# Performance work log

Hardware: AMD Instinct MI355X
Metric: run time of the kernel (lower is better)

Reference implementation:

```python
import jax, jax.numpy as jnp
import numpy as np

DIM = 1280
N_HEADS = 10
HEAD_DIM = 128
BASE = 10000.0
BATCH = 2
SEQ = 2048


def _rope(x):
    # x: [b, h, s, d]; matches source: split even/odd channels, rotate, concat halves
    b, h, s, d = x.shape
    theta = 1.0 / (BASE ** (jnp.arange(0, d, 2, dtype=jnp.float32) / d))  # [d/2]
    ang = jnp.arange(s, dtype=jnp.float32)[:, None] * theta               # [s, d/2]
    cos = jnp.cos(ang)
    sin = jnp.sin(ang)
    x1 = x[..., 0::2]
    x2 = x[..., 1::2]
    return jnp.concatenate([x1 * cos - x2 * sin, x1 * sin + x2 * cos], axis=-1)


def setup_inputs() -> dict:
    key = jax.random.key(0)
    ks = jax.random.split(key, 6)
    w_std = 0.02
    x = jax.random.normal(ks[0], (BATCH, SEQ, DIM), dtype=jnp.float32)
    positions = jnp.arange(SEQ, dtype=jnp.int64 if jax.config.jax_enable_x64 else jnp.int32)
    Wq = jax.random.normal(ks[1], (DIM, DIM), dtype=jnp.float32) * w_std
    Wk = jax.random.normal(ks[2], (DIM, DIM), dtype=jnp.float32) * w_std
    Wv = jax.random.normal(ks[3], (DIM, DIM), dtype=jnp.float32) * w_std
    Wo = jax.random.normal(ks[4], (DIM, DIM), dtype=jnp.float32) * w_std
    bq = jnp.zeros((DIM,), jnp.float32)
    bk = jnp.zeros((DIM,), jnp.float32)
    bv = jnp.zeros((DIM,), jnp.float32)
    bo = jnp.zeros((DIM,), jnp.float32)
    return {"x": x, "positions": positions, "Wq": Wq, "bq": bq, "Wk": Wk,
            "bk": bk, "Wv": Wv, "bv": bv, "Wo": Wo, "bo": bo}


def reference(x, positions, Wq, bq, Wk, bk, Wv, bv, Wo, bo):
    b, s, _ = x.shape
    scale = 1.0 / np.sqrt(HEAD_DIM)

    def proj(W, bias):
        y = jnp.einsum('bsd,ed->bse', x, W) + bias  # Linear: x @ W^T + b
        return y.reshape(b, s, N_HEADS, HEAD_DIM).transpose(0, 2, 1, 3)

    q = _rope(proj(Wq, bq))  # [b, h, s, hd]
    k = _rope(proj(Wk, bk))
    v = proj(Wv, bv)

    scores = jnp.einsum('bhqd,bhkd->bhqk', q, k) * scale
    causal = jnp.tril(jnp.ones((s, s), dtype=bool))
    scores = jnp.where(causal, scores, jnp.float32(-jnp.inf))
    attn = jax.nn.softmax(scores, axis=-1)
    out = jnp.einsum('bhqk,bhkd->bhqd', attn, v)
    out = out.transpose(0, 2, 1, 3).reshape(b, s, N_HEADS * HEAD_DIM)
    return jnp.einsum('bse,de->bsd', out, Wo) + bo
```

## Files before the change

### kernel.cpp

```cpp
#include <hip/hip_runtime.h>
#include <cmath>

typedef unsigned short u16;
typedef __attribute__((ext_vector_type(8))) short bf16x8;
typedef __attribute__((ext_vector_type(4))) float f32x4;

#define B_    2
#define SEQ_  2048
#define NH_   10
#define HD_   128
#define DIM_  1280

__device__ __forceinline__ u16 f2bf(float f) {
    union { float f; unsigned u; } v; v.f = f;
    unsigned r = (v.u + 0x7fffu + ((v.u >> 16) & 1u)) >> 16;
    return (u16)r;
}
__device__ __forceinline__ float bf2f(u16 h) {
    union { unsigned u; float f; } v; v.u = ((unsigned)h) << 16;
    return v.f;
}
__device__ __forceinline__ unsigned cvt2(float lo, float hi) {
    unsigned r;
    asm("v_cvt_pk_bf16_f32 %0, %1, %2" : "=v"(r) : "v"(lo), "v"(hi));
    return r;
}
__device__ __forceinline__ f32x4 mfma16(bf16x8 a, bf16x8 b, f32x4 c) {
    return __builtin_amdgcn_mfma_f32_16x16x32_bf16(a, b, c, 0, 0, 0);
}
__device__ __forceinline__ void g2l16(const void* g, void* l) {
    __builtin_amdgcn_global_load_lds(
        (const __attribute__((address_space(1))) unsigned*)g,
        (__attribute__((address_space(3))) unsigned*)l, 16, 0, 0);
}
__device__ __forceinline__ ushort4 pack4(float a, float b, float c, float d) {
    union { ushort4 w; unsigned u[2]; } r;
    r.u[0] = cvt2(a, b);
    r.u[1] = cvt2(c, d);
    return r.w;
}
__device__ __forceinline__ bf16x8 ldsr128(unsigned byte_off) {
    bf16x8 r;
    asm volatile("ds_read_b128 %0, %1" : "=v"(r) : "v"(byte_off));
    return r;
}
__device__ __forceinline__ unsigned lds_off(const void* p) {
    return (unsigned)(unsigned long long)
        (__attribute__((address_space(3))) const void*)p;
}

#define LGKM0() do { asm volatile("s_waitcnt lgkmcnt(0)" ::: "memory"); \
                     __builtin_amdgcn_sched_barrier(0); } while (0)
#define VMC(n)  asm volatile("s_waitcnt vmcnt(" #n ")" ::: "memory")

__global__ __launch_bounds__(256) void cvt_k(const float* __restrict__ x,
                                             const float* __restrict__ w0,
                                             const float* __restrict__ w1,
                                             const float* __restrict__ w2,
                                             const float* __restrict__ w3,
                                             u16* __restrict__ xb,
                                             u16* __restrict__ d0,
                                             u16* __restrict__ d1,
                                             u16* __restrict__ d2,
                                             u16* __restrict__ d3,
                                             float* __restrict__ ct,
                                             float* __restrict__ st) {
    const int NX = B_ * SEQ_ * DIM_;
    const int WN = DIM_ * DIM_;
    const int NCV = (NX + 4 * WN) / 8 / 256;
    int bid = blockIdx.x;
    if (bid >= NCV) {
        int idx = (bid - NCV) * 256 + threadIdx.x;
        int s = idx >> 6, j = idx & 63;
        float e = (float)j * (1.0f / 64.0f);
        float theta = 1.0f / powf(10000.0f, e);
        float ang = (float)s * theta;
        ct[idx] = cosf(ang);
        st[idx] = sinf(ang);
        return;
    }
    int i = (bid * 256 + threadIdx.x) * 8;
    const float* src; u16* dst; int off;
    if (i < NX) { src = x; dst = xb; off = i; }
    else {
        int j = i - NX; int w = j / WN; off = j - w * WN;
        src = (w == 0) ? w0 : (w == 1) ? w1 : (w == 2) ? w2 : w3;
        dst = (w == 0) ? d0 : (w == 1) ? d1 : (w == 2) ? d2 : d3;
    }
    float4 a0 = *(const float4*)(src + off);
    float4 a1 = *(const float4*)(src + off + 4);
    union { uint4 q; unsigned w[4]; } t;
    t.w[0] = cvt2(a0.x, a0.y);
    t.w[1] = cvt2(a0.z, a0.w);
    t.w[2] = cvt2(a1.x, a1.y);
    t.w[3] = cvt2(a1.z, a1.w);
    *(uint4*)(dst + off) = t.q;
}

template <typename OT>
__device__ __forceinline__ void gemm_core(const u16* __restrict__ A,
                                          const u16* __restrict__ W,
                                          const float* __restrict__ bias,
                                          OT* __restrict__ C,
                                          int m_blk, int n_blk,
                                          u16* As, u16* Bs) {
    const int tid = threadIdx.x;
    const int wave = tid >> 6, lane = tid & 63;
    const int quad = lane >> 4, l16 = lane & 15;
    const int w_m = (wave >> 1) * 64, w_n = (wave & 1) * 64;
    const int srow = wave * 32;
    const int lrow = lane >> 3;
    const int csw = ((lane & 7) ^ lrow) * 8;
    const int rsw = l16 & 7;
    f32x4 acc[4][4] = {};

    const u16* pa = A + (size_t)(m_blk + srow + lrow) * DIM_ + csw;
    const u16* pb = W + (size_t)(n_blk + srow + lrow) * DIM_ + csw;

    for (int k0 = 0; k0 < DIM_; k0 += 64) {
        #pragma unroll
        for (int i = 0; i < 4; ++i) {
            g2l16(pa + k0 + i * 8 * DIM_, As + (srow + i * 8) * 64);
            g2l16(pb + k0 + i * 8 * DIM_, Bs + (srow + i * 8) * 64);
        }
        __syncthreads();
        #pragma unroll
        for (int kk = 0; kk < 2; ++kk) {
            bf16x8 af[4], bf[4];
            #pragma unroll
            for (int mt = 0; mt < 4; ++mt)
                af[mt] = *(const bf16x8*)&As[(w_m + mt * 16 + l16) * 64
                                             + ((kk * 4 + quad) ^ rsw) * 8];
            #pragma unroll
            for (int nt = 0; nt < 4; ++nt)
                bf[nt] = *(const bf16x8*)&Bs[(w_n + nt * 16 + l16) * 64
                                             + ((kk * 4 + quad) ^ rsw) * 8];
            #pragma unroll
            for (int mt = 0; mt < 4; ++mt)
                #pragma unroll
                for (int nt = 0; nt < 4; ++nt)
                    acc[mt][nt] = mfma16(af[mt], bf[nt], acc[mt][nt]);
        }
        __syncthreads();
    }
    #pragma unroll
    for (int nt = 0; nt < 4; ++nt) {
        int col = n_blk + w_n + nt * 16 + l16;
        float bv = bias[col];
        #pragma unroll
        for (int mt = 0; mt < 4; ++mt) {
            #pragma unroll
            for (int r = 0; r < 4; ++r) {
                int row = m_blk + w_m + mt * 16 + quad * 4 + r;
                float v = acc[mt][nt][r] + bv;
                if constexpr (sizeof(OT) == 4) C[(size_t)row * DIM_ + col] = v;
                else C[(size_t)row * DIM_ + col] = (OT)f2bf(v);
            }
        }
    }
}

__device__ __forceinline__ void gemm256_core(const u16* __restrict__ A,
                                             const u16* __restrict__ W,
                                             const float* __restrict__ bias,
                                             u16* __restrict__ C,
                                             int m_blk, int n_blk,
                                             u16* sm) {
    const int tid = threadIdx.x;
    const int wave = tid >> 6, lane = tid & 63;
    const int quad = lane >> 4, l16 = lane & 15;
    const int wr = wave >> 2, wc = wave & 3;
    const int rsw = (l16 >> 1) & 3;
    const unsigned smb = lds_off(sm);
    const unsigned aB = smb + ((wr * 128 + l16) * 32 + (quad ^ rsw) * 8) * 2;
    const unsigned bB = smb + (16384 + (wc * 64 + l16) * 32 + (quad ^ rsw) * 8) * 2;
    const int csw = ((lane & 3) ^ ((lane >> 3) & 3)) * 8;
    const int jA = wave * 2, jB = wave * 2 + 1;
    const int kkA = jA >> 3, gA0 = jA & 7;
    const int kkB = jB >> 3, gB0 = jB & 7;
    const u16* pa = A + (size_t)(m_blk + (lane >> 2)) * DIM_ + csw;
    const u16* pb = W + (size_t)(n_blk + (lane >> 2)) * DIM_ + csw;

    #define STG(p, mat, d, h, tk) do {                                        \
        int g0_ = gA0 + (h) * 8, g1_ = gB0 + (h) * 8;                         \
        g2l16((p) + (size_t)(g0_ * 16) * DIM_ + (tk) * 64 + kkA * 32,         \
              sm + (d) * 32768 + (mat) * 16384 + kkA * 8192 + g0_ * 512);     \
        g2l16((p) + (size_t)(g1_ * 16) * DIM_ + (tk) * 64 + kkB * 32,         \
              sm + (d) * 32768 + (mat) * 16384 + kkB * 8192 + g1_ * 512);     \
    } while (0)

    f32x4 acc[8][4] = {};
    bf16x8 b[2][4];

    STG(pa, 0, 0, 0, 0); STG(pa, 0, 0, 1, 0);
    STG(pb, 1, 0, 0, 0); STG(pb, 1, 0, 1, 0);
    STG(pb, 1, 1, 0, 1); STG(pb, 1, 1, 1, 1);
    VMC(4);
    asm volatile("s_waitcnt lgkmcnt(0)" ::: "memory");
    __builtin_amdgcn_s_barrier();

    const int NT = DIM_ / 64;
    for (int t = 0; t < NT; ++t) {
        const unsigned cu2 = (unsigned)(t & 1) * 65536u;
        const int d = t & 1;
        const bool sa = (t + 1 < NT), sb = (t + 2 < NT);
        const unsigned aT = aB + cu2, bT = bB + cu2;
        #pragma unroll
        for (int q = 0; q < 4; ++q) {
            if (q == 0) {
                #pragma unroll
                for (int kk = 0; kk < 2; ++kk)
                    #pragma unroll
                    for (int nt = 0; nt < 4; ++nt)
                        b[kk][nt] = ldsr128(bT + (kk * 8192 + nt * 512) * 2);
            }
            bf16x8 af[2][2];
            #pragma unroll
            for (int j = 0; j < 2; ++j)
                #pragma unroll
                for (int kk = 0; kk < 2; ++kk)
                    af[j][kk] = ldsr128(aT + ((2 * q + j) * 512 + kk * 8192) * 2);
            if (q == 0 && sa) STG(pa, 0, d ^ 1, 0, t + 1);
            if (q == 1 && sa) STG(pa, 0, d ^ 1, 1, t + 1);
            if (q == 2 && sb) STG(pb, 1, d, 0, t + 2);
            if (q == 3 && sb) STG(pb, 1, d, 1, t + 2);
            if (q == 0)
                asm volatile("s_waitcnt lgkmcnt(8)" ::: "memory");
            __builtin_amdgcn_s_barrier();
            LGKM0();
            __builtin_amdgcn_s_setprio(1);
            #pragma unroll
            for (int j = 0; j < 2; ++j)
                #pragma unroll
                for (int nt = 0; nt < 4; ++nt) {
                    acc[2 * q + j][nt] = mfma16(af[j][0], b[0][nt], acc[2 * q + j][nt]);
                    acc[2 * q + j][nt] = mfma16(af[j][1], b[1][nt], acc[2 * q + j][nt]);
                }
            __builtin_amdgcn_s_setprio(0);
            if (q == 3) {
                if (sb) VMC(4);
                else if (sa) VMC(0);
            }
            __builtin_amdgcn_s_barrier();
        }
    }
    #undef STG
    #pragma unroll
    for (int nt = 0; nt < 4; ++nt) {
        int col = n_blk + wc * 64 + nt * 16 + l16;
        float bv = bias[col];
        #pragma unroll
        for (int mt = 0; mt < 8; ++mt) {
            int row = m_blk + wr * 128 + mt * 16 + quad * 4;
            #pragma unroll
            for (int r = 0; r < 4; ++r)
                C[(size_t)(row + r) * DIM_ + col] = f2bf(acc[mt][nt][r] + bv);
        }
    }
}

__global__ __launch_bounds__(512, 2) void qkv_gemm(const u16* __restrict__ xb,
                                                   const u16* __restrict__ Wqb,
                                                   const u16* __restrict__ Wkb,
                                                   const u16* __restrict__ Wvb,
                                                   const float* __restrict__ bq,
                                                   const float* __restrict__ bk,
                                                   const float* __restrict__ bv,
                                                   u16* __restrict__ Qb,
                                                   u16* __restrict__ Kb,
                                                   u16* __restrict__ Vb) {
    __shared__ alignas(16) u16 sm[65536];
    int id = blockIdx.x;
    int xcd = id & 7, pid = id >> 3;
    int m = xcd * 2 + pid / 15;
    int ns = pid % 15;
    int wsel = ns / 5, n_blk = (ns % 5) * 256;
    const u16* W = (wsel == 0) ? Wqb : (wsel == 1) ? Wkb : Wvb;
    const float* bias = (wsel == 0) ? bq : (wsel == 1) ? bk : bv;
    u16* C = (wsel == 0) ? Qb : (wsel == 1) ? Kb : Vb;
    gemm256_core(xb, W, bias, C, m * 256, n_blk, sm);
}

__global__ __launch_bounds__(256) void out_gemm(const u16* __restrict__ AO,
                                                const u16* __restrict__ Wob,
                                                const float* __restrict__ bo,
                                                float* __restrict__ C) {
    __shared__ alignas(16) u16 As[128 * 64];
    __shared__ alignas(16) u16 Bs[128 * 64];
    int id = blockIdx.x;
    int xcd = id & 7, pid = id >> 3;
    int n = pid % 10;
    int m = xcd * 4 + pid / 10;
    gemm_core<float>(AO, Wob, bo, C, m * 128, n * 128, As, Bs);
}

__global__ __launch_bounds__(256) void rope_k(const u16* __restrict__ Ks_,
                                              u16* __restrict__ Kp,
                                              const float* __restrict__ ct,
                                              const float* __restrict__ st) {
    int t = blockIdx.x * 256 + threadIdx.x;
    int rid = t >> 3, j0 = (t & 7) * 8;
    int h = rid % NH_;
    int s = (rid / NH_) % SEQ_;
    int b = rid / (NH_ * SEQ_);
    const u16* p = Ks_ + (size_t)rid * HD_ + 2 * j0;
    union { uint4 q; u16 u[8]; } a0, a1;
    a0.q = *(const uint4*)p;
    a1.q = *(const uint4*)(p + 8);
    const float* cc = ct + (size_t)s * 64 + j0;
    const float* ss = st + (size_t)s * 64 + j0;
    float y1[8], y2[8];
    #pragma unroll
    for (int j = 0; j < 8; ++j) {
        float x1 = bf2f((j < 4) ? a0.u[2 * j] : a1.u[2 * j - 8]);
        float x2 = bf2f((j < 4) ? a0.u[2 * j + 1] : a1.u[2 * j - 7]);
        float c = cc[j], sn = ss[j];
        y1[j] = x1 * c - x2 * sn;
        y2[j] = x1 * sn + x2 * c;
    }
    union { uint4 q; unsigned w[4]; } o1, o2;
    #pragma unroll
    for (int p2 = 0; p2 < 4; ++p2) {
        o1.w[p2] = cvt2(y1[2 * p2], y1[2 * p2 + 1]);
        o2.w[p2] = cvt2(y2[2 * p2], y2[2 * p2 + 1]);
    }
    int kt = s >> 6, key = s & 63, nt = key >> 4, l16k = key & 15;
    int qd = (j0 >> 3) & 3;
    int kk1 = j0 >> 5, kk2 = 2 + kk1;
    u16* tb = Kp + ((size_t)((b * NH_ + h) * 32 + kt)) * 8192;
    int lane = qd * 16 + l16k;
    *(uint4*)(tb + (kk1 * 4 + nt) * 512 + lane * 8) = o1.q;
    *(uint4*)(tb + (kk2 * 4 + nt) * 512 + lane * 8) = o2.q;
}

__global__ __launch_bounds__(256) void transpose_v(const u16* __restrict__ V,
                                                   u16* __restrict__ Vp) {
    __shared__ u16 T[128][72];
    int stile = blockIdx.x, h = blockIdx.y, b = blockIdx.z;
    int tid = threadIdx.x;
    {
        int sl = tid >> 2, d0 = (tid & 3) * 32;
        const u16* vp = V + ((size_t)((b * SEQ_ + stile * 64 + sl) * NH_ + h)) * HD_ + d0;
        #pragma unroll
        for (int i = 0; i < 4; ++i) {
            union { uint4 q; u16 u[8]; } r;
            r.q = *(const uint4*)(vp + i * 8);
            #pragma unroll
            for (int j = 0; j < 8; ++j) T[d0 + i * 8 + j][sl] = r.u[j];
        }
    }
    __syncthreads();
    {
        int d = tid >> 1, kc = (tid & 1) * 32;
        int dt = d >> 4, l16v = d & 15, kk = kc >> 5;
        u16* tb = Vp + ((size_t)((b * NH_ + h) * 32 + stile)) * 8192 + (kk * 8 + dt) * 512;
        #pragma unroll
        for (int i = 0; i < 4; ++i)
            *(uint4*)(tb + (i * 16 + l16v) * 8) = *(const uint4*)&T[d][kc + i * 8];
    }
}

__device__ const unsigned char QT_TAB[40] =
    {0,1,2,3,4,4,5,5,6,6,7,7,8,8,8,9,9,9,10,10,10,11,11,11,
     12,12,12,12,13,13,13,13,14,14,14,14,15,15,15,15};
__device__ const unsigned char CH_TAB[40] =
    {0,0,0,0,0,1,0,1,0,1,0,1,0,1,2,0,1,2,0,1,2,0,1,2,
     0,1,2,3,0,1,2,3,0,1,2,3,0,1,2,3};

__global__ __launch_bounds__(256, 3) void attn_k(const u16* Q,
                                                 const u16* __restrict__ Kp,
                                                 const u16* __restrict__ Vp,
                                                 u16* AO,
                                                 u16* __restrict__ PO,
                                                 float* __restrict__ Pl,
                                                 const float* __restrict__ ct,
                                                 const float* __restrict__ st,
                                                 float qsc) {
    const int cid = blockIdx.x, h = blockIdx.y, b = blockIdx.z;
    const int qt = QT_TAB[cid], c = CH_TAB[cid];
    const int ntiles = 2 * qt + 2;
    const int nch = (ntiles + 7) >> 3;
    const int kt0 = c * 8;
    const int kt1 = (kt0 + 8 < ntiles) ? kt0 + 8 : ntiles;
    const int bh = b * NH_ + h;

    const int tid = threadIdx.x, wave = tid >> 6, lane = tid & 63;
    const int quad = lane >> 4, l16 = lane & 15;

    __shared__ alignas(16) u16 Ks[16 * 512];
    __shared__ alignas(16) u16 Vs[16 * 512];
    __shared__ alignas(16) u16 Pt[4][4][512];

    bf16x8 qf[2][4];
    #pragma unroll
    for (int mt = 0; mt < 2; ++mt) {
        int sq = qt * 128 + wave * 32 + mt * 16 + l16;
        const u16* qp = Q + ((size_t)((b * SEQ_ + sq) * NH_ + h)) * HD_;
        const float* cc = ct + (size_t)sq * 64;
        const float* ss = st + (size_t)sq * 64;
        #pragma unroll
        for (int kk = 0; kk < 2; ++kk) {
            const int j0 = kk * 32 + quad * 8;
            union { uint4 q4; u16 u[8]; } r0, r1;
            r0.q4 = *(const uint4*)(qp + 2 * j0);
            r1.q4 = *(const uint4*)(qp + 2 * j0 + 8);
            float y1[8], y2[8];
            #pragma unroll
            for (int j = 0; j < 8; ++j) {
                float x1 = bf2f((j < 4) ? r0.u[2 * j] : r1.u[2 * j - 8]);
                float x2 = bf2f((j < 4) ? r0.u[2 * j + 1] : r1.u[2 * j - 7]);
                float cv = cc[j0 + j], sv = ss[j0 + j];
                y1[j] = (x1 * cv - x2 * sv) * qsc;
                y2[j] = (x1 * sv + x2 * cv) * qsc;
            }
            union { bf16x8 v; unsigned w[4]; } o1, o2;
            #pragma unroll
            for (int p2 = 0; p2 < 4; ++p2) {
                o1.w[p2] = cvt2(y1[2 * p2], y1[2 * p2 + 1]);
                o2.w[p2] = cvt2(y2[2 * p2], y2[2 * p2 + 1]);
            }
            qf[mt][kk] = o1.v;
            qf[mt][kk + 2] = o2.v;
        }
    }

    f32x4 oacc[2][8] = {};
    float l_run[2] = {0.f, 0.f};
    const int q0 = qt * 128 + wave * 32 + l16;

    const u16* kpb = Kp + ((size_t)bh * 32) * 8192;
    const u16* vpb = Vp + ((size_t)bh * 32) * 8192;

    for (int kt = kt0; kt < kt1; ++kt) {
        const u16* kp_t = kpb + (size_t)kt * 8192;
        const u16* vp_t = vpb + (size_t)kt * 8192;
        #pragma unroll
        for (int i = 0; i < 4; ++i) {
            int f = wave * 4 + i;
            g2l16(kp_t + f * 512 + lane * 8, &Ks[f * 512]);
            g2l16(vp_t + f * 512 + lane * 8, &Vs[f * 512]);
        }
        __syncthreads();
        f32x4 sacc[2][4] = {};
        #pragma unroll
        for (int kk = 0; kk < 4; ++kk) {
            #pragma unroll
            for (int nt = 0; nt < 4; ++nt) {
                bf16x8 kf = *(const bf16x8*)&Ks[(kk * 4 + nt) * 512 + lane * 8];
                sacc[0][nt] = mfma16(kf, qf[0][kk], sacc[0][nt]);
                sacc[1][nt] = mfma16(kf, qf[1][kk], sacc[1][nt]);
            }
        }
        const bool maskt = (kt >= 2 * qt);
        const int keyb = kt * 64 + quad * 4;
        #pragma unroll
        for (int mt = 0; mt < 2; ++mt) {
            const int qg = q0 + mt * 16;
            float ps = 0.f;
            #pragma unroll
            for (int nt = 0; nt < 4; ++nt) {
                float p[4];
                #pragma unroll
                for (int r = 0; r < 4; ++r) {
                    float x = sacc[mt][nt][r];
                    if (maskt && (keyb + nt * 16 + r > qg)) x = -INFINITY;
                    p[r] = __builtin_amdgcn_exp2f(x);
                    ps += p[r];
                }
                ushort4 w4 = pack4(p[0], p[1], p[2], p[3]);
                int rowf = (((nt & 1) << 1) | (quad >> 1)) * 16 + l16;
                *(ushort4*)&Pt[wave][mt * 2 + (nt >> 1)][rowf * 8 + (quad & 1) * 4] = w4;
            }
            l_run[mt] += ps;
        }
        #pragma unroll
        for (int kk = 0; kk < 2; ++kk) {
            bf16x8 pf0 = *(const bf16x8*)&Pt[wave][kk][(quad * 16 + l16) * 8];
            bf16x8 pf1 = *(const bf16x8*)&Pt[wave][2 + kk][(quad * 16 + l16) * 8];
            #pragma unroll
            for (int dt = 0; dt < 8; ++dt) {
                bf16x8 vf = *(const bf16x8*)&Vs[(kk * 8 + dt) * 512 + lane * 8];
                oacc[0][dt] = mfma16(vf, pf0, oacc[0][dt]);
                oacc[1][dt] = mfma16(vf, pf1, oacc[1][dt]);
            }
        }
        __syncthreads();
    }
    #pragma unroll
    for (int mt = 0; mt < 2; ++mt) {
        l_run[mt] += __shfl_xor(l_run[mt], 16, 64);
        l_run[mt] += __shfl_xor(l_run[mt], 32, 64);
    }
    if (nch == 1) {
        #pragma unroll
        for (int mt = 0; mt < 2; ++mt) {
            float invl = 1.0f / l_run[mt];
            int sq = q0 + mt * 16;
            u16* op = AO + ((size_t)((b * SEQ_ + sq) * NH_ + h)) * HD_ + quad * 4;
            #pragma unroll
            for (int dt = 0; dt < 8; ++dt) {
                ushort4 w4 = pack4(oacc[mt][dt][0] * invl, oacc[mt][dt][1] * invl,
                                   oacc[mt][dt][2] * invl, oacc[mt][dt][3] * invl);
                *(ushort4*)(op + dt * 16) = w4;
            }
        }
    } else {
        size_t pidx = ((size_t)bh * 16 + qt) * 4 + c;
        u16* po = PO + pidx * 16384;
        #pragma unroll
        for (int mt = 0; mt < 2; ++mt) {
            #pragma unroll
            for (int dt = 0; dt < 8; ++dt) {
                ushort4 w4 = pack4(oacc[mt][dt][0], oacc[mt][dt][1],
                                   oacc[mt][dt][2], oacc[mt][dt][3]);
                *(ushort4*)(po + ((wave * 16 + mt * 8 + dt) * 64 + lane) * 4) = w4;
            }
            if (quad == 0)
                Pl[pidx * 128 + wave * 32 + mt * 16 + l16] = l_run[mt];
        }
    }
}

__global__ __launch_bounds__(256) void combine_k(const u16* __restrict__ PO,
                                                 const float* __restrict__ Pl,
                                                 u16* __restrict__ AO) {
    const int qt = 4 + blockIdx.x, h = blockIdx.y, b = blockIdx.z;
    const int nch = (2 * qt + 2 + 7) >> 3;
    const int bh = b * NH_ + h;
    const int tid = threadIdx.x;
    const int q = tid >> 1, dh = tid & 1;
    const int wave = q >> 5, mt = (q >> 4) & 1, l16 = q & 15;
    size_t base = ((size_t)bh * 16 + qt) * 4;

    float L = 0.f;
    for (int c = 0; c < nch; ++c) L += Pl[(base + c) * 128 + q];
    float o[64];
    #pragma unroll
    for (int j = 0; j < 64; ++j) o[j] = 0.f;
    for (int c = 0; c < nch; ++c) {
        const u16* p = PO + (base + c) * 16384;
        #pragma unroll
        for (int dtl = 0; dtl < 4; ++dtl) {
            int dt = dh * 4 + dtl;
            #pragma unroll
            for (int quad = 0; quad < 4; ++quad) {
                union { ushort4 v; u16 u[4]; } t;
                t.v = *(const ushort4*)(p + ((wave * 16 + mt * 8 + dt) * 64
                                             + quad * 16 + l16) * 4);
                #pragma unroll
                for (int r = 0; r < 4; ++r)
                    o[dtl * 16 + quad * 4 + r] += bf2f(t.u[r]);
            }
        }
    }
    float invL = 1.0f / L;
    int sq = qt * 128 + q;
    u16* op = AO + ((size_t)((b * SEQ_ + sq) * NH_ + h)) * HD_ + dh * 64;
    union { uint4 v[8]; unsigned w[32]; } t;
    #pragma unroll
    for (int j = 0; j < 32; ++j)
        t.w[j] = cvt2(o[2 * j] * invL, o[2 * j + 1] * invL);
    #pragma unroll
    for (int i = 0; i < 8; ++i) *(uint4*)(op + i * 8) = t.v[i];
}

extern "C" void kernel_launch(void* const* d_in, const int* in_sizes, int n_in,
                              void* d_out, int out_size, void* d_ws, size_t ws_size,
                              hipStream_t stream) {
    const float* x  = (const float*)d_in[0];
    const float* Wq = (const float*)d_in[2];
    const float* bq = (const float*)d_in[3];
    const float* Wk = (const float*)d_in[4];
    const float* bk = (const float*)d_in[5];
    const float* Wv = (const float*)d_in[6];
    const float* bv = (const float*)d_in[7];
    const float* Wo = (const float*)d_in[8];
    const float* bo = (const float*)d_in[9];
    float* out = (float*)d_out;

    const size_t NE = (size_t)B_ * SEQ_ * NH_ * HD_;
    const size_t WN = (size_t)DIM_ * DIM_;
    u16* Qb  = (u16*)d_ws;
    u16* Kb  = Qb + NE;
    u16* Vb  = Kb + NE;
    u16* Vp  = Vb + NE;
    u16* xb  = Vp + NE;
    u16* Wqb = xb + NE;
    u16* Wkb = Wqb + WN;
    u16* Wvb = Wkb + WN;
    u16* Wob = Wvb + WN;
    float* ct = (float*)(Wob + WN);
    float* st = ct + (size_t)SEQ_ * 64;
    u16* PO  = (u16*)(st + (size_t)SEQ_ * 64);
    float* Pl = (float*)(PO + (size_t)B_ * NH_ * 16 * 4 * 16384);
    u16* Kp = xb;
    u16* AO = Qb;

    const int NCVT = (B_ * SEQ_ * DIM_ + 4 * (int)WN) / 8 / 256;
    cvt_k<<<NCVT + 512, 256, 0, stream>>>(x, Wq, Wk, Wv, Wo,
                                          xb, Wqb, Wkb, Wvb, Wob, ct, st);

    qkv_gemm<<<dim3(240), 512, 0, stream>>>(xb, Wqb, Wkb, Wvb, bq, bk, bv,
                                            Qb, Kb, Vb);

    transpose_v<<<dim3(SEQ_ / 64, NH_, B_), 256, 0, stream>>>(Vb, Vp);

    rope_k<<<(B_ * SEQ_ * NH_ * 8) / 256, 256, 0, stream>>>(Kb, Kp, ct, st);

    const float qsc = 0.08838834764831845f * 1.4426950408889634f;
    attn_k<<<dim3(40, NH_, B_), 256, 0, stream>>>(Qb, Kp, Vp, AO, PO, Pl,
                                                  ct, st, qsc);
    combine_k<<<dim3(12, NH_, B_), 256, 0, stream>>>(PO, Pl, AO);

    out_gemm<<<dim3(320), 256, 0, stream>>>(AO, Wob, bo, out);
}
```

Baseline: 258.1 us.

## Pipeline K/V tile loads in attention and merge V-transpose with K-rope kernel

The attention loop now preloads K and V for the first tile, then for each tile prefetches the next K tile into LDS right after QK^T and the next V tile right after PV. Waits use partial vmcnt counts and raw s_barrier instead of full __syncthreads. LDS reads are issued explicitly with ds_read_b128 and double-buffered fragment registers under partial lgkmcnt waits, and MFMA blocks are raised with s_setprio. Separately, the V transpose and K rope kernels are fused into one launch to save a kernel launch, at the cost of more register pressure and hand-counted wait logic that could be fragile.

Measured after the change: 363.6 us. 40.9% more time.

```diff
diff --git a/kernel.cpp b/kernel.cpp
--- a/kernel.cpp
+++ b/kernel.cpp
@@ -49,8 +49,9 @@
         (__attribute__((address_space(3))) const void*)p;
 }
 
-#define LGKM0() do { asm volatile("s_waitcnt lgkmcnt(0)" ::: "memory"); \
+#define LGKM(n) do { asm volatile("s_waitcnt lgkmcnt(" #n ")" ::: "memory"); \
                      __builtin_amdgcn_sched_barrier(0); } while (0)
+#define LGKM0() LGKM(0)
 #define VMC(n)  asm volatile("s_waitcnt vmcnt(" #n ")" ::: "memory")
 
 __global__ __launch_bounds__(256) void cvt_k(const float* __restrict__ x,
@@ -294,11 +295,40 @@
     gemm_core<float>(AO, Wob, bo, C, m * 128, n * 128, As, Bs);
 }
 
-__global__ __launch_bounds__(256) void rope_k(const u16* __restrict__ Ks_,
-                                              u16* __restrict__ Kp,
-                                              const float* __restrict__ ct,
-                                              const float* __restrict__ st) {
-    int t = blockIdx.x * 256 + threadIdx.x;
+__global__ __launch_bounds__(256) void pack_kv(const u16* __restrict__ V,
+                                               u16* __restrict__ Vp,
+                                               const u16* __restrict__ Ks_,
+                                               u16* __restrict__ Kp,
+                                               const float* __restrict__ ct,
+                                               const float* __restrict__ st) {
+    int bid = blockIdx.x;
+    int tid = threadIdx.x;
+    if (bid < 640) {
+        __shared__ u16 T[128][72];
+        int stile = bid & 31, h = (bid >> 5) % NH_, b = bid / 320;
+        {
+            int sl = tid >> 2, d0 = (tid & 3) * 32;
+            const u16* vp = V + ((size_t)((b * SEQ_ + stile * 64 + sl) * NH_ + h)) * HD_ + d0;
+            #pragma unroll
+            for (int i = 0; i < 4; ++i) {
+                union { uint4 q; u16 u[8]; } r;
+                r.q = *(const uint4*)(vp + i * 8);
+                #pragma unroll
+                for (int j = 0; j < 8; ++j) T[d0 + i * 8 + j][sl] = r.u[j];
+            }
+        }
+        __syncthreads();
+        {
+            int d = tid >> 1, kc = (tid & 1) * 32;
+            int dt = d >> 4, l16v = d & 15, kk = kc >> 5;
+            u16* tb = Vp + ((size_t)((b * NH_ + h) * 32 + stile)) * 8192 + (kk * 8 + dt) * 512;
+            #pragma unroll
+            for (int i = 0; i < 4; ++i)
+                *(uint4*)(tb + (i * 16 + l16v) * 8) = *(const uint4*)&T[d][kc + i * 8];
+        }
+        return;
+    }
+    int t = (bid - 640) * 256 + tid;
     int rid = t >> 3, j0 = (t & 7) * 8;
     int h = rid % NH_;
     int s = (rid / NH_) % SEQ_;
@@ -331,33 +361,6 @@
     int lane = qd * 16 + l16k;
     *(uint4*)(tb + (kk1 * 4 + nt) * 512 + lane * 8) = o1.q;
     *(uint4*)(tb + (kk2 * 4 + nt) * 512 + lane * 8) = o2.q;
-}
-
-__global__ __launch_bounds__(256) void transpose_v(const u16* __restrict__ V,
-                                                   u16* __restrict__ Vp) {
-    __shared__ u16 T[128][72];
-    int stile = blockIdx.x, h = blockIdx.y, b = blockIdx.z;
-    int tid = threadIdx.x;
-    {
-        int sl = tid >> 2, d0 = (tid & 3) * 32;
-        const u16* vp = V + ((size_t)((b * SEQ_ + stile * 64 + sl) * NH_ + h)) * HD_ + d0;
-        #pragma unroll
-        for (int i = 0; i < 4; ++i) {
-            union { uint4 q; u16 u[8]; } r;
-            r.q = *(const uint4*)(vp + i * 8);
-            #pragma unroll
-            for (int j = 0; j < 8; ++j) T[d0 + i * 8 + j][sl] = r.u[j];
-        }
-    }
-    __syncthreads();
-    {
-        int d = tid >> 1, kc = (tid & 1) * 32;
-        int dt = d >> 4, l16v = d & 15, kk = kc >> 5;
-        u16* tb = Vp + ((size_t)((b * NH_ + h) * 32 + stile)) * 8192 + (kk * 8 + dt) * 512;
-        #pragma unroll
-        for (int i = 0; i < 4; ++i)
-            *(uint4*)(tb + (i * 16 + l16v) * 8) = *(const uint4*)&T[d][kc + i * 8];
-    }
 }
 
 __device__ const unsigned char QT_TAB[40] =
@@ -430,25 +433,64 @@
 
     const u16* kpb = Kp + ((size_t)bh * 32) * 8192;
     const u16* vpb = Vp + ((size_t)bh * 32) * 8192;
-
-    for (int kt = kt0; kt < kt1; ++kt) {
-        const u16* kp_t = kpb + (size_t)kt * 8192;
-        const u16* vp_t = vpb + (size_t)kt * 8192;
+    const unsigned ksb = lds_off(Ks);
+    const unsigned vsb = lds_off(Vs);
+    const unsigned ptb = lds_off(&Pt[wave][0][0]);
+
+    {
+        const u16* kp_t = kpb + (size_t)kt0 * 8192;
+        const u16* vp_t = vpb + (size_t)kt0 * 8192;
         #pragma unroll
         for (int i = 0; i < 4; ++i) {
             int f = wave * 4 + i;
             g2l16(kp_t + f * 512 + lane * 8, &Ks[f * 512]);
+        }
+        #pragma unroll
+        for (int i = 0; i < 4; ++i) {
+            int f = wave * 4 + i;
             g2l16(vp_t + f * 512 + lane * 8, &Vs[f * 512]);
         }
-        __syncthreads();
+    }
+
+    for (int kt = kt0; kt < kt1; ++kt) {
+        const bool more = (kt + 1 < kt1);
+        VMC(4);
+        __builtin_amdgcn_s_barrier();
         f32x4 sacc[2][4] = {};
-        #pragma unroll
-        for (int kk = 0; kk < 4; ++kk) {
-            #pragma unroll
-            for (int nt = 0; nt < 4; ++nt) {
-                bf16x8 kf = *(const bf16x8*)&Ks[(kk * 4 + nt) * 512 + lane * 8];
-                sacc[0][nt] = mfma16(kf, qf[0][kk], sacc[0][nt]);
-                sacc[1][nt] = mfma16(kf, qf[1][kk], sacc[1][nt]);
+        {
+            bf16x8 kfA[4], kfB[4];
+            #pragma unroll
+            for (int nt = 0; nt < 4; ++nt)
+                kfA[nt] = ldsr128(ksb + ((0 * 4 + nt) * 512 + lane * 8) * 2);
+            #pragma unroll
+            for (int kk = 0; kk < 4; ++kk) {
+                if (kk < 3) {
+                    #pragma unroll
+                    for (int nt = 0; nt < 4; ++nt) {
+                        bf16x8 v = ldsr128(ksb + (((kk + 1) * 4 + nt) * 512 + lane * 8) * 2);
+                        if (kk & 1) kfA[nt] = v; else kfB[nt] = v;
+                    }
+                    LGKM(4);
+                } else {
+                    LGKM(0);
+                }
+                __builtin_amdgcn_s_setprio(1);
+                #pragma unroll
+                for (int nt = 0; nt < 4; ++nt) {
+                    bf16x8 kf = (kk & 1) ? kfB[nt] : kfA[nt];
+                    sacc[0][nt] = mfma16(kf, qf[0][kk], sacc[0][nt]);
+                    sacc[1][nt] = mfma16(kf, qf[1][kk], sacc[1][nt]);
+                }
+                __builtin_amdgcn_s_setprio(0);
+            }
+        }
+        __builtin_amdgcn_s_barrier();
+        if (more) {
+            const u16* kp_n = kpb + (size_t)(kt + 1) * 8192;
+            #pragma unroll
+            for (int i = 0; i < 4; ++i) {
+                int f = wave * 4 + i;
+                g2l16(kp_n + f * 512 + lane * 8, &Ks[f * 512]);
             }
         }
         const bool maskt = (kt >= 2 * qt);
@@ -473,18 +515,34 @@
             }
             l_run[mt] += ps;
         }
+        if (more) VMC(4); else VMC(0);
+        __builtin_amdgcn_s_barrier();
         #pragma unroll
         for (int kk = 0; kk < 2; ++kk) {
-            bf16x8 pf0 = *(const bf16x8*)&Pt[wave][kk][(quad * 16 + l16) * 8];
-            bf16x8 pf1 = *(const bf16x8*)&Pt[wave][2 + kk][(quad * 16 + l16) * 8];
+            bf16x8 pf0 = ldsr128(ptb + ((kk) * 512 + (quad * 16 + l16) * 8) * 2);
+            bf16x8 pf1 = ldsr128(ptb + ((2 + kk) * 512 + (quad * 16 + l16) * 8) * 2);
+            bf16x8 vf[8];
+            #pragma unroll
+            for (int dt = 0; dt < 8; ++dt)
+                vf[dt] = ldsr128(vsb + ((kk * 8 + dt) * 512 + lane * 8) * 2);
+            LGKM(0);
+            __builtin_amdgcn_s_setprio(1);
             #pragma unroll
             for (int dt = 0; dt < 8; ++dt) {
-                bf16x8 vf = *(const bf16x8*)&Vs[(kk * 8 + dt) * 512 + lane * 8];
-                oacc[0][dt] = mfma16(vf, pf0, oacc[0][dt]);
-                oacc[1][dt] = mfma16(vf, pf1, oacc[1][dt]);
-            }
-        }
-        __syncthreads();
+                oacc[0][dt] = mfma16(vf[dt], pf0, oacc[0][dt]);
+                oacc[1][dt] = mfma16(vf[dt], pf1, oacc[1][dt]);
+            }
+            __builtin_amdgcn_s_setprio(0);
+        }
+        __builtin_amdgcn_s_barrier();
+        if (more) {
+            const u16* vp_n = vpb + (size_t)(kt + 1) * 8192;
+            #pragma unroll
+            for (int i = 0; i < 4; ++i) {
+                int f = wave * 4 + i;
+                g2l16(vp_n + f * 512 + lane * 8, &Vs[f * 512]);
+            }
+        }
     }
     #pragma unroll
     for (int mt = 0; mt < 2; ++mt) {
@@ -603,9 +661,7 @@
     qkv_gemm<<<dim3(240), 512, 0, stream>>>(xb, Wqb, Wkb, Wvb, bq, bk, bv,
                                             Qb, Kb, Vb);
 
-    transpose_v<<<dim3(SEQ_ / 64, NH_, B_), 256, 0, stream>>>(Vb, Vp);
-
-    rope_k<<<(B_ * SEQ_ * NH_ * 8) / 256, 256, 0, stream>>>(Kb, Kp, ct, st);
+    pack_kv<<<dim3(640 + 1280), 256, 0, stream>>>(Vb, Vp, Kb, Kp, ct, st);
 
     const float qsc = 0.08838834764831845f * 1.4426950408889634f;
     attn_k<<<dim3(40, NH_, B_), 256, 0, stream>>>(Qb, Kp, Vp, AO, PO, Pl,
```
